# Optimization experiments

Hardware: AMD Instinct MI355X
Metric: run time of the kernel (lower is better)

## Reference

```python
import jax, jax.numpy as jnp
import numpy as np

N, C, H, W = 8, 64, 128, 128
K2 = 9  # 3x3 kernel
BN_EPS = 1e-5


def conv3x3(x, w):
    # x: [N,Ci,H,W], w: [Co,Ci,3,3], stride 1, padding 1, dilation 1
    return jax.lax.conv_general_dilated(
        x, w, window_strides=(1, 1), padding=((1, 1), (1, 1)),
        dimension_numbers=('NCHW', 'OIHW', 'NCHW'))


def deform_conv3x3(x, offset, w):
    # torchvision deform_conv2d v1 (no mask), stride 1, pad 1, dil 1, 1 group.
    # offset: [N, 2*K2, H, W] ordered (dy, dx) per kernel tap.
    n, c, h, wd = x.shape
    off = offset.reshape(n, K2, 2, h, wd)
    k = jnp.arange(3) - 1  # kernel tap displacements with pad=1
    ky, kx = jnp.meshgrid(k, k, indexing='ij')
    ky = ky.reshape(K2).astype(x.dtype)
    kx = kx.reshape(K2).astype(x.dtype)
    ys = jnp.arange(h, dtype=x.dtype)
    xs = jnp.arange(wd, dtype=x.dtype)
    # sampling positions: [N, K2, H, W]
    py = ys[None, None, :, None] + ky[None, :, None, None] + off[:, :, 0]
    px = xs[None, None, None, :] + kx[None, :, None, None] + off[:, :, 1]
    y0f = jnp.floor(py)
    x0f = jnp.floor(px)
    wy1 = py - y0f
    wx1 = px - x0f
    y0 = y0f.astype(jnp.int32)
    x0 = x0f.astype(jnp.int32)
    xflat = x.reshape(n, c, h * wd)

    def corner(yc, xc, wgt):
        valid = ((yc >= 0) & (yc < h) & (xc >= 0) & (xc < wd)).astype(x.dtype)
        idx = jnp.clip(yc, 0, h - 1) * wd + jnp.clip(xc, 0, wd - 1)  # [N,K2,H,W]
        gath = jax.vmap(lambda xf, i: jnp.take(xf, i.reshape(-1), axis=1)
                        .reshape(c, K2, h, wd))(xflat, idx)  # [N,C,K2,H,W]
        return gath * (wgt * valid)[:, None]

    samp = (corner(y0, x0, (1 - wy1) * (1 - wx1))
            + corner(y0, x0 + 1, (1 - wy1) * wx1)
            + corner(y0 + 1, x0, wy1 * (1 - wx1))
            + corner(y0 + 1, x0 + 1, wy1 * wx1))  # [N,C,K2,H,W]
    return jnp.einsum('nckhw,ock->nohw', samp, w.reshape(w.shape[0], c, K2))


def setup_inputs() -> dict:
    key = jax.random.key(0)
    ks = jax.random.split(key, 5)
    x = jax.random.normal(ks[0], (N, C, H, W), dtype=jnp.float32)
    # small offset-conv weights so predicted offsets stay within a few pixels
    w_off = jax.random.normal(ks[1], (2 * K2 + 9, C, 3, 3), dtype=jnp.float32) * 0.01
    w_def = jax.random.normal(ks[2], (C, C, 3, 3), dtype=jnp.float32) * (1.0 / np.sqrt(C * 9))
    w1 = jax.random.normal(ks[3], (K2, C, 3, 3), dtype=jnp.float32) * (1.0 / np.sqrt(C * 9))
    gamma = jnp.ones((K2,), jnp.float32)
    beta = jnp.zeros((K2,), jnp.float32)
    mean = jnp.zeros((K2,), jnp.float32)
    var = jnp.ones((K2,), jnp.float32)
    return {"x": x, "w_off": w_off, "w_def": w_def, "w1": w1,
            "gamma": gamma, "beta": beta, "mean": mean, "var": var}


def reference(x, w_off, w_def, w1, gamma, beta, mean, var):
    off_filter = conv3x3(x, w_off)            # [N, 27, H, W]
    offset = off_filter[:, :2 * K2]           # [N, 18, H, W]
    filt = off_filter[:, -K2:]                # [N, 9, H, W]
    out = deform_conv3x3(x, offset, w_def)    # [N, C, H, W]
    xr = x + out
    h = conv3x3(xr, w1)                       # [N, 9, H, W]
    # BatchNorm2d (inference form with running stats)
    h = (h - mean[None, :, None, None]) * jax.lax.rsqrt(var[None, :, None, None] + BN_EPS)
    h = h * gamma[None, :, None, None] + beta[None, :, None, None]
    h = jnp.maximum(h, 0.0)
    return (h, filt)
```

## Files before the change

kernel.cpp:

```cpp
#include <hip/hip_runtime.h>
#include <hip/hip_bf16.h>
#include <cmath>

#define H_ 128
#define W_ 128
#define HW_ 16384
#define C_ 64
#define N_ 8
#define BN_EPS 1e-5f

typedef __attribute__((ext_vector_type(8))) short short8;
typedef __attribute__((ext_vector_type(4))) float float4_;
typedef __attribute__((ext_vector_type(4))) unsigned uint4_;
typedef __attribute__((ext_vector_type(2))) unsigned uint2_;

__device__ inline short f2bf(float f) {
    unsigned u = __builtin_bit_cast(unsigned, f);
    u += 0x7fffu + ((u >> 16) & 1u);
    return (short)(u >> 16);
}
__device__ inline float bf2f(short s) {
    unsigned u = ((unsigned)(unsigned short)s) << 16;
    return __builtin_bit_cast(float, u);
}
__device__ inline unsigned pkbf2(float a, float b) {
    __hip_bfloat162 h = __float22bfloat162_rn(make_float2(a, b));
    unsigned u;
    __builtin_memcpy(&u, &h, 4);
    return u;
}
__device__ inline float bperm_f(int addr, float v) {
    return __builtin_bit_cast(float,
        __builtin_amdgcn_ds_bpermute(addr, __builtin_bit_cast(int, v)));
}
__device__ inline float bfu_lo(unsigned u) {
    return __builtin_bit_cast(float, u << 16);
}
__device__ inline float bfu_hi(unsigned u) {
    return __builtin_bit_cast(float, u & 0xffff0000u);
}

#if __has_builtin(__builtin_amdgcn_fdot2_f32_bf16)
#define HAS_FDOT2 1
typedef __bf16 bf16x2v __attribute__((ext_vector_type(2)));
__device__ inline float fdot2bf(unsigned a, unsigned b, float c) {
    return __builtin_amdgcn_fdot2_f32_bf16(
        __builtin_bit_cast(bf16x2v, a), __builtin_bit_cast(bf16x2v, b), c, false);
}
#else
#define HAS_FDOT2 0
#endif

#define XR8_OFS    0
#define WDEFB_OFS  16777216
#define BT27_OFS   16850944
#define BT9_OFS    16888320

#define PS_ 402

__global__ __launch_bounds__(256) void prep_w(
    const float* __restrict__ w_off, const float* __restrict__ w_def,
    const float* __restrict__ w1, short* __restrict__ wdefB,
    short* __restrict__ bt27, short* __restrict__ bt9)
{
    int i = blockIdx.x * 256 + threadIdx.x;
    if (i < 36864) {
        int o = i / 576, r = i - o*576, t = r >> 6, c = r & 63;
        wdefB[i] = f2bf(w_def[o*576 + c*9 + t]);
    } else if (i < 36864 + 18688) {
        int j = i - 36864;
        int oc = j / 584, K = j - oc*584;
        float v = 0.f;
        if (oc < 27 && K < 576) { int t = K >> 6, c = K & 63; v = w_off[oc*576 + c*9 + t]; }
        bt27[j] = f2bf(v);
    } else if (i < 36864 + 18688 + 9344) {
        int j = i - 36864 - 18688;
        int oc = j / 584, K = j - oc*584;
        float v = 0.f;
        if (oc < 9 && K < 576) { int t = K >> 6, c = K & 63; v = w1[oc*576 + c*9 + t]; }
        bt9[j] = f2bf(v);
    }
}

__global__ __launch_bounds__(256, 2) void fused_off_deform(
    const float* __restrict__ x, const short8* __restrict__ btg27,
    const short8* __restrict__ wdefB, float* __restrict__ filt_out,
    short* __restrict__ xr8s)
{
    __shared__ short8 patch[8*PS_];
    const int tid = threadIdx.x;
    const int bx = blockIdx.x, by = blockIdx.y, n = blockIdx.z;
    const int lane = tid & 63, wid = tid >> 6;
    const int q = lane >> 4, col = lane & 15;
    const int r0 = by*16 - 2, c0 = bx*16 - 2;
    const float* xb = x + (size_t)n * C_ * HW_;

    for (int i = tid; i < 3200; i += 256) {
        int c8 = i / 400, r = i - c8*400;
        int py = r / 20, px = r - py*20;
        int gy = r0 + py, gx = c0 + px;
        uint4_ u = (uint4_){0u,0u,0u,0u};
        if ((unsigned)gy < 128u && (unsigned)gx < 128u) {
            const float* xp = xb + (size_t)(c8*8)*HW_ + gy*W_ + gx;
            u[0] = pkbf2(xp[0],      xp[HW_]);
            u[1] = pkbf2(xp[2*HW_],  xp[3*HW_]);
            u[2] = pkbf2(xp[4*HW_],  xp[5*HW_]);
            u[3] = pkbf2(xp[6*HW_],  xp[7*HW_]);
        }
        patch[c8*PS_ + py*20 + px] = __builtin_bit_cast(short8, u);
    }
    __syncthreads();

    float4_ a27[2][4];
    #pragma unroll
    for (int m = 0; m < 2; m++)
        #pragma unroll
        for (int i = 0; i < 4; i++) a27[m][i] = (float4_){0.f,0.f,0.f,0.f};

    #pragma unroll 2
    for (int k0 = 0; k0 < 18; k0++) {
        int t = k0 >> 1;
        int dy = t/3, dx = t - dy*3;
        int c8 = (k0 & 1)*4 + q;
        short8 w0 = btg27[col*73 + k0*4 + q];
        short8 w1 = btg27[(16 + col)*73 + k0*4 + q];
        #pragma unroll
        for (int i = 0; i < 4; i++) {
            int mt = wid*4 + i;
            short8 p = patch[c8*PS_ + (mt + dy + 1)*20 + (col + dx + 1)];
            a27[0][i] = __builtin_amdgcn_mfma_f32_16x16x32_bf16(w0, p, a27[0][i], 0,0,0);
            a27[1][i] = __builtin_amdgcn_mfma_f32_16x16x32_bf16(w1, p, a27[1][i], 0,0,0);
        }
    }

    #pragma unroll
    for (int i = 0; i < 4; i++) {
        int prow = by*16 + wid*4 + i;
        #pragma unroll
        for (int reg = 0; reg < 4; reg++) {
            int oc = 16 + q*4 + reg;
            if (oc >= 18 && oc < 27)
                filt_out[((size_t)n*9 + (oc-18))*HW_ + prow*W_ + bx*16 + col] = a27[1][i][reg];
        }
    }

    float4_ acc[4][4];
    #pragma unroll
    for (int i = 0; i < 4; i++)
        #pragma unroll
        for (int nt = 0; nt < 4; nt++) acc[i][nt] = (float4_){0.f,0.f,0.f,0.f};

    const int col4 = col*4;
    const int gxc = bx*16 + col;

    auto tap = [&](int t, int dy, int dx, const float* oy, const float* ox) {
        short8 afrag[4][2];
        #pragma unroll
        for (int i = 0; i < 4; i++) {
            const int gy = by*16 + wid*4 + i;
            float py = (float)(gy + dy) + oy[i];
            float px = (float)(gxc + dx) + ox[i];
            float y0f = floorf(py), x0f = floorf(px);
            float wy1 = py - y0f, wx1 = px - x0f;
            float wy0 = 1.f - wy1, wx0 = 1.f - wx1;
            int y0 = (int)y0f, x0 = (int)x0f;
            int y1 = y0 + 1,   x1 = x0 + 1;
            float wy0v = ((unsigned)y0 < (unsigned)H_) ? wy0 : 0.f;
            float wy1v = ((unsigned)y1 < (unsigned)H_) ? wy1 : 0.f;
            float wx0v = ((unsigned)x0 < (unsigned)W_) ? wx0 : 0.f;
            float wx1v = ((unsigned)x1 < (unsigned)W_) ? wx1 : 0.f;
            float w00 = wy0v*wx0v, w01 = wy0v*wx1v;
            float w10 = wy1v*wx0v, w11 = wy1v*wx1v;
            int cy0 = min(max(y0, 0), H_-1), cy1 = min(max(y1, 0), H_-1);
            int cx0 = min(max(x0, 0), W_-1), cx1 = min(max(x1, 0), W_-1);
            int ly0 = cy0 - r0, ly1 = cy1 - r0;
            int lx0 = cx0 - c0, lx1 = cx1 - c0;
            bool inp = ((unsigned)ly0 < 20u) & ((unsigned)ly1 < 20u)
                     & ((unsigned)lx0 < 20u) & ((unsigned)lx1 < 20u);
#if HAS_FDOT2
            unsigned w01pk = pkbf2(w00, w01);
            unsigned w23pk = pkbf2(w10, w11);
#endif
            #pragma unroll
            for (int ks = 0; ks < 2; ks++) {
                const int c8 = ks*4 + q;
                uint4_ u;
                if (inp) {
                    const short8* pl = &patch[c8*PS_];
                    short8 p00 = pl[ly0*20 + lx0], p01 = pl[ly0*20 + lx1];
                    short8 p10 = pl[ly1*20 + lx0], p11 = pl[ly1*20 + lx1];
#if HAS_FDOT2
                    uint4_ u00 = __builtin_bit_cast(uint4_, p00);
                    uint4_ u01 = __builtin_bit_cast(uint4_, p01);
                    uint4_ u10 = __builtin_bit_cast(uint4_, p10);
                    uint4_ u11 = __builtin_bit_cast(uint4_, p11);
                    #pragma unroll
                    for (int d = 0; d < 4; d++) {
                        unsigned lo01 = __builtin_amdgcn_perm(u01[d], u00[d], 0x05040100u);
                        unsigned hi01 = __builtin_amdgcn_perm(u01[d], u00[d], 0x07060302u);
                        unsigned lo23 = __builtin_amdgcn_perm(u11[d], u10[d], 0x05040100u);
                        unsigned hi23 = __builtin_amdgcn_perm(u11[d], u10[d], 0x07060302u);
                        float slo = fdot2bf(lo01, w01pk, fdot2bf(lo23, w23pk, 0.f));
                        float shi = fdot2bf(hi01, w01pk, fdot2bf(hi23, w23pk, 0.f));
                        u[d] = pkbf2(slo, shi);
                    }
#else
                    float s[8];
                    #pragma unroll
                    for (int j = 0; j < 8; j++)
                        s[j] = bf2f(p00[j])*w00 + bf2f(p01[j])*w01
                             + bf2f(p10[j])*w10 + bf2f(p11[j])*w11;
                    u[0] = pkbf2(s[0],s[1]); u[1] = pkbf2(s[2],s[3]);
                    u[2] = pkbf2(s[4],s[5]); u[3] = pkbf2(s[6],s[7]);
#endif
                } else {
                    const float* xg = xb + (size_t)(c8*8)*HW_;
                    float s[8];
                    #pragma unroll
                    for (int j = 0; j < 8; j++) {
                        const float* xj = xg + (size_t)j*HW_;
                        s[j] = xj[cy0*W_+cx0]*w00 + xj[cy0*W_+cx1]*w01
                             + xj[cy1*W_+cx0]*w10 + xj[cy1*W_+cx1]*w11;
                    }
                    u[0] = pkbf2(s[0],s[1]); u[1] = pkbf2(s[2],s[3]);
                    u[2] = pkbf2(s[4],s[5]); u[3] = pkbf2(s[6],s[7]);
                }
                afrag[i][ks] = __builtin_bit_cast(short8, u);
            }
        }
        #pragma unroll
        for (int ks = 0; ks < 2; ks++) {
            #pragma unroll
            for (int nt = 0; nt < 4; nt++) {
                short8 b = wdefB[(size_t)(nt*16 + col)*72 + t*8 + ks*4 + q];
                #pragma unroll
                for (int i = 0; i < 4; i++)
                    acc[i][nt] = __builtin_amdgcn_mfma_f32_16x16x32_bf16(
                        b, afrag[i][ks], acc[i][nt], 0,0,0);
            }
        }
    };

    {
        float oy8[4], ox8[4];
        #pragma unroll
        for (int i = 0; i < 4; i++) {
            oy8[i] = bperm_f(col4, a27[1][i][0]);
            ox8[i] = bperm_f(col4, a27[1][i][1]);
        }
        tap(8, 1, 1, oy8, ox8);
    }
    #pragma unroll 1
    for (int tp = 0; tp < 4; tp++) {
        const int addr = (tp << 6) + col4;
        float oyA[4], oxA[4], oyB[4], oxB[4];
        #pragma unroll
        for (int i = 0; i < 4; i++) {
            oyA[i] = bperm_f(addr, a27[0][i][0]);
            oxA[i] = bperm_f(addr, a27[0][i][1]);
            oyB[i] = bperm_f(addr, a27[0][i][2]);
            oxB[i] = bperm_f(addr, a27[0][i][3]);
        }
        const int tA = 2*tp, tB = 2*tp + 1;
        tap(tA, tA/3 - 1, (tA - (tA/3)*3) - 1, oyA, oxA);
        tap(tB, tB/3 - 1, (tB - (tB/3)*3) - 1, oyB, oxB);
    }

    const short* ps = (const short*)patch;
    short* xout = xr8s + (size_t)n*8*HW_*8;
    const int inner = (q & 1) * 4;
    #pragma unroll
    for (int i = 0; i < 4; i++) {
        const int row = wid*4 + i;
        const int pix = (by*16 + row)*W_ + bx*16 + col;
        #pragma unroll
        for (int nt = 0; nt < 4; nt++) {
            const int c8 = 2*nt + (q >> 1);
            const unsigned* pw = (const unsigned*)(ps
                + ((c8*PS_ + (row+2)*20 + (col+2)) << 3) + inner);
            unsigned r0w = pw[0], r1w = pw[1];
            float v0 = acc[i][nt][0] + bfu_lo(r0w);
            float v1 = acc[i][nt][1] + bfu_hi(r0w);
            float v2 = acc[i][nt][2] + bfu_lo(r1w);
            float v3 = acc[i][nt][3] + bfu_hi(r1w);
            uint2_ o2 = (uint2_){ pkbf2(v0, v1), pkbf2(v2, v3) };
            *(uint2_*)(xout + (((size_t)c8*HW_ + pix) << 3) + inner) = o2;
        }
    }
}

__global__ __launch_bounds__(256) void conv9_mfma(
    const short8* __restrict__ xr8, const short8* __restrict__ btg,
    const float* __restrict__ gamma, const float* __restrict__ beta,
    const float* __restrict__ mean, const float* __restrict__ var,
    float* __restrict__ out)
{
    __shared__ short8 patch[8*325];
    const int tid = threadIdx.x;
    const int bx = blockIdx.x, by = blockIdx.y, n = blockIdx.z;

    for (int i = tid; i < 2592; i += 256) {
        int c8 = i / 324, r = i - c8*324;
        int py = r / 18, px = r - py*18;
        int gy = by*16 - 1 + py, gx = bx*16 - 1 + px;
        short8 v = {0,0,0,0,0,0,0,0};
        if ((unsigned)gy < 128u && (unsigned)gx < 128u)
            v = xr8[(size_t)(n*8 + c8)*HW_ + gy*W_ + gx];
        patch[c8*325 + py*18 + px] = v;
    }
    __syncthreads();

    const int lane = tid & 63, wid = tid >> 6;
    const int q = lane >> 4, col = lane & 15;
    float4_ acc[4];
    #pragma unroll
    for (int i = 0; i < 4; i++) acc[i] = (float4_){0.f,0.f,0.f,0.f};

    #pragma unroll 6
    for (int k0 = 0; k0 < 18; k0++) {
        int t = k0 >> 1;
        int dy = t/3, dx = t - dy*3;
        int c8 = (k0 & 1)*4 + q;
        short8 b0 = btg[col*73 + k0*4 + q];
        #pragma unroll
        for (int i = 0; i < 4; i++) {
            int mt = wid*4 + i;
            short8 a = patch[c8*325 + (mt + dy)*18 + (col + dx)];
            acc[i] = __builtin_amdgcn_mfma_f32_16x16x32_bf16(a, b0, acc[i], 0,0,0);
        }
    }

    float sc = 0.f, sh = 0.f;
    if (col < 9) {
        sc = gamma[col] * rsqrtf(var[col] + BN_EPS);
        sh = beta[col] - mean[col] * sc;
    }
    #pragma unroll
    for (int i = 0; i < 4; i++) {
        int mt = wid*4 + i;
        if (col < 9) {
            int pix0 = (by*16 + mt)*W_ + bx*16 + q*4;
            float4_ v;
            #pragma unroll
            for (int reg = 0; reg < 4; reg++)
                v[reg] = fmaxf(fmaf(acc[i][reg], sc, sh), 0.f);
            *(float4_*)&out[((size_t)n*9 + col)*HW_ + pix0] = v;
        }
    }
}

extern "C" void kernel_launch(void* const* d_in, const int* in_sizes, int n_in,
                              void* d_out, int out_size, void* d_ws, size_t ws_size,
                              hipStream_t stream)
{
    const float* x     = (const float*)d_in[0];
    const float* w_off = (const float*)d_in[1];
    const float* w_def = (const float*)d_in[2];
    const float* w1    = (const float*)d_in[3];
    const float* gamma = (const float*)d_in[4];
    const float* beta  = (const float*)d_in[5];
    const float* mean  = (const float*)d_in[6];
    const float* var   = (const float*)d_in[7];
    float* out = (float*)d_out;

    char* ws = (char*)d_ws;
    short8* xr8     = (short8*)(ws + XR8_OFS);
    short*  wdefB   = (short*)(ws + WDEFB_OFS);
    short*  bt27    = (short*)(ws + BT27_OFS);
    short*  bt9     = (short*)(ws + BT9_OFS);

    float* h_out    = out;
    float* filt_out = out + (size_t)N_ * 9 * HW_;

    prep_w<<<dim3(254), dim3(256), 0, stream>>>(w_off, w_def, w1, wdefB, bt27, bt9);

    dim3 cgrid(8, 8, 8);
    fused_off_deform<<<cgrid, dim3(256), 0, stream>>>(
        x, (const short8*)bt27, (const short8*)wdefB, filt_out, (short*)xr8);
    conv9_mfma<<<cgrid, dim3(256), 0, stream>>>(
        xr8, (const short8*)bt9, gamma, beta, mean, var, h_out);
}
```

Measured before the change: 157.6 us.

## Merge three kernels into one persistent kernel with atomic grid barriers

Folds the weight-prep, the fused offset/deformable conv and the final 3x3 conv+BN+ReLU kernels into a single launch of 512 blocks, separated by two global atomic-counter grid barriers. The barrier counter is zeroed with a memset before launch. This removes two kernel launch gaps and their tail effects. In exchange it adds spin-wait barrier cost, and it needs all 512 blocks to be co-resident, which relies on occupancy (2 blocks/CU across the available CUs) to avoid deadlock.

```diff
diff --git a/kernel.cpp b/kernel.cpp
--- a/kernel.cpp
+++ b/kernel.cpp
@@ -8,6 +8,7 @@
 #define C_ 64
 #define N_ 8
 #define BN_EPS 1e-5f
+#define NBLOCKS_ 512u
 
 typedef __attribute__((ext_vector_type(8))) short short8;
 typedef __attribute__((ext_vector_type(4))) float float4_;
@@ -55,296 +56,313 @@
 #define WDEFB_OFS  16777216
 #define BT27_OFS   16850944
 #define BT9_OFS    16888320
+#define BAR_OFS    16907264
 
 #define PS_ 402
-
-__global__ __launch_bounds__(256) void prep_w(
-    const float* __restrict__ w_off, const float* __restrict__ w_def,
-    const float* __restrict__ w1, short* __restrict__ wdefB,
-    short* __restrict__ bt27, short* __restrict__ bt9)
-{
-    int i = blockIdx.x * 256 + threadIdx.x;
-    if (i < 36864) {
-        int o = i / 576, r = i - o*576, t = r >> 6, c = r & 63;
-        wdefB[i] = f2bf(w_def[o*576 + c*9 + t]);
-    } else if (i < 36864 + 18688) {
-        int j = i - 36864;
-        int oc = j / 584, K = j - oc*584;
-        float v = 0.f;
-        if (oc < 27 && K < 576) { int t = K >> 6, c = K & 63; v = w_off[oc*576 + c*9 + t]; }
-        bt27[j] = f2bf(v);
-    } else if (i < 36864 + 18688 + 9344) {
-        int j = i - 36864 - 18688;
-        int oc = j / 584, K = j - oc*584;
-        float v = 0.f;
-        if (oc < 9 && K < 576) { int t = K >> 6, c = K & 63; v = w1[oc*576 + c*9 + t]; }
-        bt9[j] = f2bf(v);
+#define C9PS 325
+
+__device__ inline void gridbar(unsigned* c) {
+    __syncthreads();
+    if (threadIdx.x == 0) {
+        __hip_atomic_fetch_add(c, 1u, __ATOMIC_ACQ_REL, __HIP_MEMORY_SCOPE_AGENT);
+        while (__hip_atomic_load(c, __ATOMIC_ACQUIRE, __HIP_MEMORY_SCOPE_AGENT)
+               < NBLOCKS_) {
+            __builtin_amdgcn_s_sleep(2);
+        }
     }
-}
-
-__global__ __launch_bounds__(256, 2) void fused_off_deform(
-    const float* __restrict__ x, const short8* __restrict__ btg27,
-    const short8* __restrict__ wdefB, float* __restrict__ filt_out,
-    short* __restrict__ xr8s)
+    __syncthreads();
+}
+
+__global__ __launch_bounds__(256, 2) void mega(
+    const float* __restrict__ x, const float* __restrict__ w_off,
+    const float* __restrict__ w_def, const float* __restrict__ w1,
+    const float* __restrict__ gamma, const float* __restrict__ beta,
+    const float* __restrict__ mean, const float* __restrict__ var,
+    short* __restrict__ wdefB_s, short* __restrict__ bt27_s,
+    short* __restrict__ bt9_s, short* __restrict__ xr8s,
+    float* __restrict__ filt_out, float* __restrict__ h_out,
+    unsigned* bar)
 {
     __shared__ short8 patch[8*PS_];
     const int tid = threadIdx.x;
     const int bx = blockIdx.x, by = blockIdx.y, n = blockIdx.z;
+    const int bid = (n*8 + by)*8 + bx;
+
+    {
+        int i = bid*256 + tid;
+        if (i < 36864) {
+            int o = i / 576, r = i - o*576, t = r >> 6, c = r & 63;
+            wdefB_s[i] = f2bf(w_def[o*576 + c*9 + t]);
+        } else if (i < 36864 + 18688) {
+            int j = i - 36864;
+            int oc = j / 584, K = j - oc*584;
+            float v = 0.f;
+            if (oc < 27 && K < 576) { int t = K >> 6, c = K & 63; v = w_off[oc*576 + c*9 + t]; }
+            bt27_s[j] = f2bf(v);
+        } else if (i < 36864 + 18688 + 9344) {
+            int j = i - 36864 - 18688;
+            int oc = j / 584, K = j - oc*584;
+            float v = 0.f;
+            if (oc < 9 && K < 576) { int t = K >> 6, c = K & 63; v = w1[oc*576 + c*9 + t]; }
+            bt9_s[j] = f2bf(v);
+        }
+    }
+    gridbar(&bar[0]);
+
+    const short8* btg27 = (const short8*)bt27_s;
+    const short8* wdefB = (const short8*)wdefB_s;
     const int lane = tid & 63, wid = tid >> 6;
     const int q = lane >> 4, col = lane & 15;
-    const int r0 = by*16 - 2, c0 = bx*16 - 2;
-    const float* xb = x + (size_t)n * C_ * HW_;
-
-    for (int i = tid; i < 3200; i += 256) {
-        int c8 = i / 400, r = i - c8*400;
-        int py = r / 20, px = r - py*20;
-        int gy = r0 + py, gx = c0 + px;
-        uint4_ u = (uint4_){0u,0u,0u,0u};
-        if ((unsigned)gy < 128u && (unsigned)gx < 128u) {
-            const float* xp = xb + (size_t)(c8*8)*HW_ + gy*W_ + gx;
-            u[0] = pkbf2(xp[0],      xp[HW_]);
-            u[1] = pkbf2(xp[2*HW_],  xp[3*HW_]);
-            u[2] = pkbf2(xp[4*HW_],  xp[5*HW_]);
-            u[3] = pkbf2(xp[6*HW_],  xp[7*HW_]);
-        }
-        patch[c8*PS_ + py*20 + px] = __builtin_bit_cast(short8, u);
+
+    {
+        const int r0 = by*16 - 2, c0 = bx*16 - 2;
+        const float* xb = x + (size_t)n * C_ * HW_;
+
+        for (int i = tid; i < 3200; i += 256) {
+            int c8 = i / 400, r = i - c8*400;
+            int py = r / 20, px = r - py*20;
+            int gy = r0 + py, gx = c0 + px;
+            uint4_ u = (uint4_){0u,0u,0u,0u};
+            if ((unsigned)gy < 128u && (unsigned)gx < 128u) {
+                const float* xp = xb + (size_t)(c8*8)*HW_ + gy*W_ + gx;
+                u[0] = pkbf2(xp[0],      xp[HW_]);
+                u[1] = pkbf2(xp[2*HW_],  xp[3*HW_]);
+                u[2] = pkbf2(xp[4*HW_],  xp[5*HW_]);
+                u[3] = pkbf2(xp[6*HW_],  xp[7*HW_]);
+            }
+            patch[c8*PS_ + py*20 + px] = __builtin_bit_cast(short8, u);
+        }
+        __syncthreads();
+
+        float4_ a27[2][4];
+        #pragma unroll
+        for (int m = 0; m < 2; m++)
+            #pragma unroll
+            for (int i = 0; i < 4; i++) a27[m][i] = (float4_){0.f,0.f,0.f,0.f};
+
+        #pragma unroll 2
+        for (int k0 = 0; k0 < 18; k0++) {
+            int t = k0 >> 1;
+            int dy = t/3, dx = t - dy*3;
+            int c8 = (k0 & 1)*4 + q;
+            short8 w0 = btg27[col*73 + k0*4 + q];
+            short8 w1f = btg27[(16 + col)*73 + k0*4 + q];
+            #pragma unroll
+            for (int i = 0; i < 4; i++) {
+                int mt = wid*4 + i;
+                short8 p = patch[c8*PS_ + (mt + dy + 1)*20 + (col + dx + 1)];
+                a27[0][i] = __builtin_amdgcn_mfma_f32_16x16x32_bf16(w0,  p, a27[0][i], 0,0,0);
+                a27[1][i] = __builtin_amdgcn_mfma_f32_16x16x32_bf16(w1f, p, a27[1][i], 0,0,0);
+            }
+        }
+
+        #pragma unroll
+        for (int i = 0; i < 4; i++) {
+            int prow = by*16 + wid*4 + i;
+            #pragma unroll
+            for (int reg = 0; reg < 4; reg++) {
+                int oc = 16 + q*4 + reg;
+                if (oc >= 18 && oc < 27)
+                    filt_out[((size_t)n*9 + (oc-18))*HW_ + prow*W_ + bx*16 + col] = a27[1][i][reg];
+            }
+        }
+
+        float4_ acc[4][4];
+        #pragma unroll
+        for (int i = 0; i < 4; i++)
+            #pragma unroll
+            for (int nt = 0; nt < 4; nt++) acc[i][nt] = (float4_){0.f,0.f,0.f,0.f};
+
+        const int col4 = col*4;
+        const int gxc = bx*16 + col;
+
+        auto tap = [&](int t, int dy, int dx, const float* oy, const float* ox) {
+            short8 afrag[4][2];
+            #pragma unroll
+            for (int i = 0; i < 4; i++) {
+                const int gy = by*16 + wid*4 + i;
+                float py = (float)(gy + dy) + oy[i];
+                float px = (float)(gxc + dx) + ox[i];
+                float y0f = floorf(py), x0f = floorf(px);
+                float wy1 = py - y0f, wx1 = px - x0f;
+                float wy0 = 1.f - wy1, wx0 = 1.f - wx1;
+                int y0 = (int)y0f, x0 = (int)x0f;
+                int y1 = y0 + 1,   x1 = x0 + 1;
+                float wy0v = ((unsigned)y0 < (unsigned)H_) ? wy0 : 0.f;
+                float wy1v = ((unsigned)y1 < (unsigned)H_) ? wy1 : 0.f;
+                float wx0v = ((unsigned)x0 < (unsigned)W_) ? wx0 : 0.f;
+                float wx1v = ((unsigned)x1 < (unsigned)W_) ? wx1 : 0.f;
+                float w00 = wy0v*wx0v, w01 = wy0v*wx1v;
+                float w10 = wy1v*wx0v, w11 = wy1v*wx1v;
+                int cy0 = min(max(y0, 0), H_-1), cy1 = min(max(y1, 0), H_-1);
+                int cx0 = min(max(x0, 0), W_-1), cx1 = min(max(x1, 0), W_-1);
+                int ly0 = cy0 - r0, ly1 = cy1 - r0;
+                int lx0 = cx0 - c0, lx1 = cx1 - c0;
+                bool inp = ((unsigned)ly0 < 20u) & ((unsigned)ly1 < 20u)
+                         & ((unsigned)lx0 < 20u) & ((unsigned)lx1 < 20u);
+#if HAS_FDOT2
+                unsigned w01pk = pkbf2(w00, w01);
+                unsigned w23pk = pkbf2(w10, w11);
+#endif
+                #pragma unroll
+                for (int ks = 0; ks < 2; ks++) {
+                    const int c8 = ks*4 + q;
+                    uint4_ u;
+                    if (inp) {
+                        const short8* pl = &patch[c8*PS_];
+                        short8 p00 = pl[ly0*20 + lx0], p01 = pl[ly0*20 + lx1];
+                        short8 p10 = pl[ly1*20 + lx0], p11 = pl[ly1*20 + lx1];
+#if HAS_FDOT2
+                        uint4_ u00 = __builtin_bit_cast(uint4_, p00);
+                        uint4_ u01 = __builtin_bit_cast(uint4_, p01);
+                        uint4_ u10 = __builtin_bit_cast(uint4_, p10);
+                        uint4_ u11 = __builtin_bit_cast(uint4_, p11);
+                        #pragma unroll
+                        for (int d = 0; d < 4; d++) {
+                            unsigned lo01 = __builtin_amdgcn_perm(u01[d], u00[d], 0x05040100u);
+                            unsigned hi01 = __builtin_amdgcn_perm(u01[d], u00[d], 0x07060302u);
+                            unsigned lo23 = __builtin_amdgcn_perm(u11[d], u10[d], 0x05040100u);
+                            unsigned hi23 = __builtin_amdgcn_perm(u11[d], u10[d], 0x07060302u);
+                            float slo = fdot2bf(lo01, w01pk, fdot2bf(lo23, w23pk, 0.f));
+                            float shi = fdot2bf(hi01, w01pk, fdot2bf(hi23, w23pk, 0.f));
+                            u[d] = pkbf2(slo, shi);
+                        }
+#else
+                        float s[8];
+                        #pragma unroll
+                        for (int j = 0; j < 8; j++)
+                            s[j] = bf2f(p00[j])*w00 + bf2f(p01[j])*w01
+                                 + bf2f(p10[j])*w10 + bf2f(p11[j])*w11;
+                        u[0] = pkbf2(s[0],s[1]); u[1] = pkbf2(s[2],s[3]);
+                        u[2] = pkbf2(s[4],s[5]); u[3] = pkbf2(s[6],s[7]);
+#endif
+                    } else {
+                        const float* xg = xb + (size_t)(c8*8)*HW_;
+                        float s[8];
+                        #pragma unroll
+                        for (int j = 0; j < 8; j++) {
+                            const float* xj = xg + (size_t)j*HW_;
+                            s[j] = xj[cy0*W_+cx0]*w00 + xj[cy0*W_+cx1]*w01
+                                 + xj[cy1*W_+cx0]*w10 + xj[cy1*W_+cx1]*w11;
+                        }
+                        u[0] = pkbf2(s[0],s[1]); u[1] = pkbf2(s[2],s[3]);
+                        u[2] = pkbf2(s[4],s[5]); u[3] = pkbf2(s[6],s[7]);
+                    }
+                    afrag[i][ks] = __builtin_bit_cast(short8, u);
+                }
+            }
+            #pragma unroll
+            for (int ks = 0; ks < 2; ks++) {
+                #pragma unroll
+                for (int nt = 0; nt < 4; nt++) {
+                    short8 b = wdefB[(size_t)(nt*16 + col)*72 + t*8 + ks*4 + q];
+                    #pragma unroll
+                    for (int i = 0; i < 4; i++)
+                        acc[i][nt] = __builtin_amdgcn_mfma_f32_16x16x32_bf16(
+                            b, afrag[i][ks], acc[i][nt], 0,0,0);
+                }
+            }
+        };
+
+        {
+            float oy8[4], ox8[4];
+            #pragma unroll
+            for (int i = 0; i < 4; i++) {
+                oy8[i] = bperm_f(col4, a27[1][i][0]);
+                ox8[i] = bperm_f(col4, a27[1][i][1]);
+            }
+            tap(8, 1, 1, oy8, ox8);
+        }
+        #pragma unroll 1
+        for (int tp = 0; tp < 4; tp++) {
+            const int addr = (tp << 6) + col4;
+            float oyA[4], oxA[4], oyB[4], oxB[4];
+            #pragma unroll
+            for (int i = 0; i < 4; i++) {
+                oyA[i] = bperm_f(addr, a27[0][i][0]);
+                oxA[i] = bperm_f(addr, a27[0][i][1]);
+                oyB[i] = bperm_f(addr, a27[0][i][2]);
+                oxB[i] = bperm_f(addr, a27[0][i][3]);
+            }
+            const int tA = 2*tp, tB = 2*tp + 1;
+            tap(tA, tA/3 - 1, (tA - (tA/3)*3) - 1, oyA, oxA);
+            tap(tB, tB/3 - 1, (tB - (tB/3)*3) - 1, oyB, oxB);
+        }
+
+        const short* ps = (const short*)patch;
+        short* xout = xr8s + (size_t)n*8*HW_*8;
+        const int inner = (q & 1) * 4;
+        #pragma unroll
+        for (int i = 0; i < 4; i++) {
+            const int row = wid*4 + i;
+            const int pix = (by*16 + row)*W_ + bx*16 + col;
+            #pragma unroll
+            for (int nt = 0; nt < 4; nt++) {
+                const int c8 = 2*nt + (q >> 1);
+                const unsigned* pw = (const unsigned*)(ps
+                    + ((c8*PS_ + (row+2)*20 + (col+2)) << 3) + inner);
+                unsigned r0w = pw[0], r1w = pw[1];
+                float v0 = acc[i][nt][0] + bfu_lo(r0w);
+                float v1 = acc[i][nt][1] + bfu_hi(r0w);
+                float v2 = acc[i][nt][2] + bfu_lo(r1w);
+                float v3 = acc[i][nt][3] + bfu_hi(r1w);
+                uint2_ o2 = (uint2_){ pkbf2(v0, v1), pkbf2(v2, v3) };
+                *(uint2_*)(xout + (((size_t)c8*HW_ + pix) << 3) + inner) = o2;
+            }
+        }
     }
-    __syncthreads();
-
-    float4_ a27[2][4];
-    #pragma unroll
-    for (int m = 0; m < 2; m++)
-        #pragma unroll
-        for (int i = 0; i < 4; i++) a27[m][i] = (float4_){0.f,0.f,0.f,0.f};
-
-    #pragma unroll 2
-    for (int k0 = 0; k0 < 18; k0++) {
-        int t = k0 >> 1;
-        int dy = t/3, dx = t - dy*3;
-        int c8 = (k0 & 1)*4 + q;
-        short8 w0 = btg27[col*73 + k0*4 + q];
-        short8 w1 = btg27[(16 + col)*73 + k0*4 + q];
+
+    gridbar(&bar[1]);
+
+    {
+        const short8* xr8 = (const short8*)xr8s;
+        const short8* btg = (const short8*)bt9_s;
+
+        for (int i = tid; i < 2592; i += 256) {
+            int c8 = i / 324, r = i - c8*324;
+            int py = r / 18, px = r - py*18;
+            int gy = by*16 - 1 + py, gx = bx*16 - 1 + px;
+            short8 v = {0,0,0,0,0,0,0,0};
+            if ((unsigned)gy < 128u && (unsigned)gx < 128u)
+                v = xr8[(size_t)(n*8 + c8)*HW_ + gy*W_ + gx];
+            patch[c8*C9PS + py*18 + px] = v;
+        }
+        __syncthreads();
+
+        float4_ acc[4];
+        #pragma unroll
+        for (int i = 0; i < 4; i++) acc[i] = (float4_){0.f,0.f,0.f,0.f};
+
+        #pragma unroll 6
+        for (int k0 = 0; k0 < 18; k0++) {
+            int t = k0 >> 1;
+            int dy = t/3, dx = t - dy*3;
+            int c8 = (k0 & 1)*4 + q;
+            short8 b0 = btg[col*73 + k0*4 + q];
+            #pragma unroll
+            for (int i = 0; i < 4; i++) {
+                int mt = wid*4 + i;
+                short8 a = patch[c8*C9PS + (mt + dy)*18 + (col + dx)];
+                acc[i] = __builtin_amdgcn_mfma_f32_16x16x32_bf16(a, b0, acc[i], 0,0,0);
+            }
+        }
+
+        float sc = 0.f, sh = 0.f;
+        if (col < 9) {
+            sc = gamma[col] * rsqrtf(var[col] + BN_EPS);
+            sh = beta[col] - mean[col] * sc;
+        }
         #pragma unroll
         for (int i = 0; i < 4; i++) {
             int mt = wid*4 + i;
-            short8 p = patch[c8*PS_ + (mt + dy + 1)*20 + (col + dx + 1)];
-            a27[0][i] = __builtin_amdgcn_mfma_f32_16x16x32_bf16(w0, p, a27[0][i], 0,0,0);
-            a27[1][i] = __builtin_amdgcn_mfma_f32_16x16x32_bf16(w1, p, a27[1][i], 0,0,0);
-        }
-    }
-
-    #pragma unroll
-    for (int i = 0; i < 4; i++) {
-        int prow = by*16 + wid*4 + i;
-        #pragma unroll
-        for (int reg = 0; reg < 4; reg++) {
-            int oc = 16 + q*4 + reg;
-            if (oc >= 18 && oc < 27)
-                filt_out[((size_t)n*9 + (oc-18))*HW_ + prow*W_ + bx*16 + col] = a27[1][i][reg];
-        }
-    }
-
-    float4_ acc[4][4];
-    #pragma unroll
-    for (int i = 0; i < 4; i++)
-        #pragma unroll
-        for (int nt = 0; nt < 4; nt++) acc[i][nt] = (float4_){0.f,0.f,0.f,0.f};
-
-    const int col4 = col*4;
-    const int gxc = bx*16 + col;
-
-    auto tap = [&](int t, int dy, int dx, const float* oy, const float* ox) {
-        short8 afrag[4][2];
-        #pragma unroll
-        for (int i = 0; i < 4; i++) {
-            const int gy = by*16 + wid*4 + i;
-            float py = (float)(gy + dy) + oy[i];
-            float px = (float)(gxc + dx) + ox[i];
-            float y0f = floorf(py), x0f = floorf(px);
-            float wy1 = py - y0f, wx1 = px - x0f;
-            float wy0 = 1.f - wy1, wx0 = 1.f - wx1;
-            int y0 = (int)y0f, x0 = (int)x0f;
-            int y1 = y0 + 1,   x1 = x0 + 1;
-            float wy0v = ((unsigned)y0 < (unsigned)H_) ? wy0 : 0.f;
-            float wy1v = ((unsigned)y1 < (unsigned)H_) ? wy1 : 0.f;
-            float wx0v = ((unsigned)x0 < (unsigned)W_) ? wx0 : 0.f;
-            float wx1v = ((unsigned)x1 < (unsigned)W_) ? wx1 : 0.f;
-            float w00 = wy0v*wx0v, w01 = wy0v*wx1v;
-            float w10 = wy1v*wx0v, w11 = wy1v*wx1v;
-            int cy0 = min(max(y0, 0), H_-1), cy1 = min(max(y1, 0), H_-1);
-            int cx0 = min(max(x0, 0), W_-1), cx1 = min(max(x1, 0), W_-1);
-            int ly0 = cy0 - r0, ly1 = cy1 - r0;
-            int lx0 = cx0 - c0, lx1 = cx1 - c0;
-            bool inp = ((unsigned)ly0 < 20u) & ((unsigned)ly1 < 20u)
-                     & ((unsigned)lx0 < 20u) & ((unsigned)lx1 < 20u);
-#if HAS_FDOT2
-            unsigned w01pk = pkbf2(w00, w01);
-            unsigned w23pk = pkbf2(w10, w11);
-#endif
-            #pragma unroll
-            for (int ks = 0; ks < 2; ks++) {
-                const int c8 = ks*4 + q;
-                uint4_ u;
-                if (inp) {
-                    const short8* pl = &patch[c8*PS_];
-                    short8 p00 = pl[ly0*20 + lx0], p01 = pl[ly0*20 + lx1];
-                    short8 p10 = pl[ly1*20 + lx0], p11 = pl[ly1*20 + lx1];
-#if HAS_FDOT2
-                    uint4_ u00 = __builtin_bit_cast(uint4_, p00);
-                    uint4_ u01 = __builtin_bit_cast(uint4_, p01);
-                    uint4_ u10 = __builtin_bit_cast(uint4_, p10);
-                    uint4_ u11 = __builtin_bit_cast(uint4_, p11);
-                    #pragma unroll
-                    for (int d = 0; d < 4; d++) {
-                        unsigned lo01 = __builtin_amdgcn_perm(u01[d], u00[d], 0x05040100u);
-                        unsigned hi01 = __builtin_amdgcn_perm(u01[d], u00[d], 0x07060302u);
-                        unsigned lo23 = __builtin_amdgcn_perm(u11[d], u10[d], 0x05040100u);
-                        unsigned hi23 = __builtin_amdgcn_perm(u11[d], u10[d], 0x07060302u);
-                        float slo = fdot2bf(lo01, w01pk, fdot2bf(lo23, w23pk, 0.f));
-                        float shi = fdot2bf(hi01, w01pk, fdot2bf(hi23, w23pk, 0.f));
-                        u[d] = pkbf2(slo, shi);
-                    }
-#else
-                    float s[8];
-                    #pragma unroll
-                    for (int j = 0; j < 8; j++)
-                        s[j] = bf2f(p00[j])*w00 + bf2f(p01[j])*w01
-                             + bf2f(p10[j])*w10 + bf2f(p11[j])*w11;
-                    u[0] = pkbf2(s[0],s[1]); u[1] = pkbf2(s[2],s[3]);
-                    u[2] = pkbf2(s[4],s[5]); u[3] = pkbf2(s[6],s[7]);
-#endif
-                } else {
-                    const float* xg = xb + (size_t)(c8*8)*HW_;
-                    float s[8];
-                    #pragma unroll
-                    for (int j = 0; j < 8; j++) {
-                        const float* xj = xg + (size_t)j*HW_;
-                        s[j] = xj[cy0*W_+cx0]*w00 + xj[cy0*W_+cx1]*w01
-                             + xj[cy1*W_+cx0]*w10 + xj[cy1*W_+cx1]*w11;
-                    }
-                    u[0] = pkbf2(s[0],s[1]); u[1] = pkbf2(s[2],s[3]);
-                    u[2] = pkbf2(s[4],s[5]); u[3] = pkbf2(s[6],s[7]);
-                }
-                afrag[i][ks] = __builtin_bit_cast(short8, u);
-            }
-        }
-        #pragma unroll
-        for (int ks = 0; ks < 2; ks++) {
-            #pragma unroll
-            for (int nt = 0; nt < 4; nt++) {
-                short8 b = wdefB[(size_t)(nt*16 + col)*72 + t*8 + ks*4 + q];
+            if (col < 9) {
+                int pix0 = (by*16 + mt)*W_ + bx*16 + q*4;
+                float4_ v;
                 #pragma unroll
-                for (int i = 0; i < 4; i++)
-                    acc[i][nt] = __builtin_amdgcn_mfma_f32_16x16x32_bf16(
-                        b, afrag[i][ks], acc[i][nt], 0,0,0);
-            }
-        }
-    };
-
-    {
-        float oy8[4], ox8[4];
-        #pragma unroll
-        for (int i = 0; i < 4; i++) {
-            oy8[i] = bperm_f(col4, a27[1][i][0]);
-            ox8[i] = bperm_f(col4, a27[1][i][1]);
-        }
-        tap(8, 1, 1, oy8, ox8);
-    }
-    #pragma unroll 1
-    for (int tp = 0; tp < 4; tp++) {
-        const int addr = (tp << 6) + col4;
-        float oyA[4], oxA[4], oyB[4], oxB[4];
-        #pragma unroll
-        for (int i = 0; i < 4; i++) {
-            oyA[i] = bperm_f(addr, a27[0][i][0]);
-            oxA[i] = bperm_f(addr, a27[0][i][1]);
-            oyB[i] = bperm_f(addr, a27[0][i][2]);
-            oxB[i] = bperm_f(addr, a27[0][i][3]);
-        }
-        const int tA = 2*tp, tB = 2*tp + 1;
-        tap(tA, tA/3 - 1, (tA - (tA/3)*3) - 1, oyA, oxA);
-        tap(tB, tB/3 - 1, (tB - (tB/3)*3) - 1, oyB, oxB);
-    }
-
-    const short* ps = (const short*)patch;
-    short* xout = xr8s + (size_t)n*8*HW_*8;
-    const int inner = (q & 1) * 4;
-    #pragma unroll
-    for (int i = 0; i < 4; i++) {
-        const int row = wid*4 + i;
-        const int pix = (by*16 + row)*W_ + bx*16 + col;
-        #pragma unroll
-        for (int nt = 0; nt < 4; nt++) {
-            const int c8 = 2*nt + (q >> 1);
-            const unsigned* pw = (const unsigned*)(ps
-                + ((c8*PS_ + (row+2)*20 + (col+2)) << 3) + inner);
-            unsigned r0w = pw[0], r1w = pw[1];
-            float v0 = acc[i][nt][0] + bfu_lo(r0w);
-            float v1 = acc[i][nt][1] + bfu_hi(r0w);
-            float v2 = acc[i][nt][2] + bfu_lo(r1w);
-            float v3 = acc[i][nt][3] + bfu_hi(r1w);
-            uint2_ o2 = (uint2_){ pkbf2(v0, v1), pkbf2(v2, v3) };
-            *(uint2_*)(xout + (((size_t)c8*HW_ + pix) << 3) + inner) = o2;
-        }
-    }
-}
-
-__global__ __launch_bounds__(256) void conv9_mfma(
-    const short8* __restrict__ xr8, const short8* __restrict__ btg,
-    const float* __restrict__ gamma, const float* __restrict__ beta,
-    const float* __restrict__ mean, const float* __restrict__ var,
-    float* __restrict__ out)
-{
-    __shared__ short8 patch[8*325];
-    const int tid = threadIdx.x;
-    const int bx = blockIdx.x, by = blockIdx.y, n = blockIdx.z;
-
-    for (int i = tid; i < 2592; i += 256) {
-        int c8 = i / 324, r = i - c8*324;
-        int py = r / 18, px = r - py*18;
-        int gy = by*16 - 1 + py, gx = bx*16 - 1 + px;
-        short8 v = {0,0,0,0,0,0,0,0};
-        if ((unsigned)gy < 128u && (unsigned)gx < 128u)
-            v = xr8[(size_t)(n*8 + c8)*HW_ + gy*W_ + gx];
-        patch[c8*325 + py*18 + px] = v;
-    }
-    __syncthreads();
-
-    const int lane = tid & 63, wid = tid >> 6;
-    const int q = lane >> 4, col = lane & 15;
-    float4_ acc[4];
-    #pragma unroll
-    for (int i = 0; i < 4; i++) acc[i] = (float4_){0.f,0.f,0.f,0.f};
-
-    #pragma unroll 6
-    for (int k0 = 0; k0 < 18; k0++) {
-        int t = k0 >> 1;
-        int dy = t/3, dx = t - dy*3;
-        int c8 = (k0 & 1)*4 + q;
-        short8 b0 = btg[col*73 + k0*4 + q];
-        #pragma unroll
-        for (int i = 0; i < 4; i++) {
-            int mt = wid*4 + i;
-            short8 a = patch[c8*325 + (mt + dy)*18 + (col + dx)];
-            acc[i] = __builtin_amdgcn_mfma_f32_16x16x32_bf16(a, b0, acc[i], 0,0,0);
-        }
-    }
-
-    float sc = 0.f, sh = 0.f;
-    if (col < 9) {
-        sc = gamma[col] * rsqrtf(var[col] + BN_EPS);
-        sh = beta[col] - mean[col] * sc;
-    }
-    #pragma unroll
-    for (int i = 0; i < 4; i++) {
-        int mt = wid*4 + i;
-        if (col < 9) {
-            int pix0 = (by*16 + mt)*W_ + bx*16 + q*4;
-            float4_ v;
-            #pragma unroll
-            for (int reg = 0; reg < 4; reg++)
-                v[reg] = fmaxf(fmaf(acc[i][reg], sc, sh), 0.f);
-            *(float4_*)&out[((size_t)n*9 + col)*HW_ + pix0] = v;
+                for (int reg = 0; reg < 4; reg++)
+                    v[reg] = fmaxf(fmaf(acc[i][reg], sc, sh), 0.f);
+                *(float4_*)&h_out[((size_t)n*9 + col)*HW_ + pix0] = v;
+            }
         }
     }
 }
@@ -364,19 +382,18 @@
     float* out = (float*)d_out;
 
     char* ws = (char*)d_ws;
-    short8* xr8     = (short8*)(ws + XR8_OFS);
-    short*  wdefB   = (short*)(ws + WDEFB_OFS);
-    short*  bt27    = (short*)(ws + BT27_OFS);
-    short*  bt9     = (short*)(ws + BT9_OFS);
+    short* xr8    = (short*)(ws + XR8_OFS);
+    short* wdefB  = (short*)(ws + WDEFB_OFS);
+    short* bt27   = (short*)(ws + BT27_OFS);
+    short* bt9    = (short*)(ws + BT9_OFS);
+    unsigned* bar = (unsigned*)(ws + BAR_OFS);
 
     float* h_out    = out;
     float* filt_out = out + (size_t)N_ * 9 * HW_;
 
-    prep_w<<<dim3(254), dim3(256), 0, stream>>>(w_off, w_def, w1, wdefB, bt27, bt9);
-
-    dim3 cgrid(8, 8, 8);
-    fused_off_deform<<<cgrid, dim3(256), 0, stream>>>(
-        x, (const short8*)bt27, (const short8*)wdefB, filt_out, (short*)xr8);
-    conv9_mfma<<<cgrid, dim3(256), 0, stream>>>(
-        xr8, (const short8*)bt9, gamma, beta, mean, var, h_out);
-}
+    hipMemsetAsync((void*)bar, 0, 64, stream);
+
+    mega<<<dim3(8, 8, 8), dim3(256), 0, stream>>>(
+        x, w_off, w_def, w1, gamma, beta, mean, var,
+        wdefB, bt27, bt9, xr8, filt_out, h_out, bar);
+}
```

After: 237.4 us. 50.7% more time.
